# Kernel optimization log

Hardware: AMD Instinct MI355X
Metric: run time of the kernel (lower is better)

Reference implementation:

```python
import jax, jax.numpy as jnp
import numpy as np

B, S, H = 1, 1024, 2048          # batch, seq, hidden_size
I = 7168                          # intermediate_size
E = 8                             # num_local_experts
TOP_K = 2                         # num_experts_per_tok
R = int(I * H * 0.1 / (I + H))    # delta_low_rank = 159
SCALE = 0.02


def setup_inputs() -> dict:
    key = jax.random.key(0)
    ks = jax.random.split(key, 12)
    f = jnp.float32
    return {
        "x": jax.random.normal(ks[0], (B, S, H), dtype=f),
        "gate_w": jax.random.normal(ks[1], (E, H), dtype=f) * SCALE,
        "Wm1": jax.random.normal(ks[2], (I, H), dtype=f) * SCALE,  # Wmean1 (gate proj)
        "Wm2": jax.random.normal(ks[3], (H, I), dtype=f) * SCALE,  # Wmean2 (down proj)
        "Wm3": jax.random.normal(ks[4], (I, H), dtype=f) * SCALE,  # Wmean3 (up proj)
        "du1": jax.random.normal(ks[5], (E, I, R), dtype=f) * SCALE,
        "dv1": jax.random.normal(ks[6], (E, R, H), dtype=f) * SCALE,
        "du2": jax.random.normal(ks[7], (E, H, R), dtype=f) * SCALE,
        "dv2": jax.random.normal(ks[8], (E, R, I), dtype=f) * SCALE,
        "du3": jax.random.normal(ks[9], (E, I, R), dtype=f) * SCALE,
        "dv3": jax.random.normal(ks[10], (E, R, H), dtype=f) * SCALE,
    }


def reference(x, gate_w, Wm1, Wm2, Wm3, du1, dv1, du2, dv2, du3, dv3):
    b, s, h = x.shape
    hs = x.reshape(-1, h)                                  # [T, H]

    # --- router ---
    router_logits = hs @ gate_w.T                          # [T, E]
    probs = jax.nn.softmax(router_logits.astype(jnp.float32), axis=-1)
    top_w, top_i = jax.lax.top_k(probs, TOP_K)             # [T, K]
    top_w = top_w / jnp.sum(top_w, axis=-1, keepdims=True)
    # dense combine weights [T, E]: weight of expert e for token t (0 if not selected)
    comb = jnp.sum(jax.nn.one_hot(top_i, E, dtype=top_w.dtype) * top_w[..., None], axis=1)
    comb = comb.astype(hs.dtype)

    # --- shared mean weights (computed once per token) ---
    base_gate = hs @ Wm1.T                                 # [T, I]
    base_up = hs @ Wm3.T                                   # [T, I]

    # --- per-expert low-rank deltas ---
    t1 = jnp.einsum('th,erh->ter', hs, dv1)                # [T, E, R]
    gate = base_gate[:, None, :] + jnp.einsum('ter,eir->tei', t1, du1)  # [T, E, I]
    t3 = jnp.einsum('th,erh->ter', hs, dv3)
    up = base_up[:, None, :] + jnp.einsum('ter,eir->tei', t3, du3)      # [T, E, I]

    hmid = jax.nn.silu(gate) * up                          # [T, E, I]

    out = jnp.einsum('tei,hi->teh', hmid, Wm2)             # shared down proj
    t2 = jnp.einsum('tei,eri->ter', hmid, dv2)
    out = out + jnp.einsum('ter,ehr->teh', t2, du2)        # [T, E, H]

    final = jnp.einsum('te,teh->th', comb, out).reshape(b, s, h)
    return final, router_logits
```

## Files before the change

kernel.cpp:

```cpp
#include <hip/hip_runtime.h>

#define T_TOK 1024
#define H_DIM 2048
#define I_DIM 7168
#define E_NUM 8
#define R_RANK 159
#define RP 160
#define P_PAIRS 2048

#define CH_X    262144L
#define CH_W    1835008L
#define CH_DV13 325632L
#define CH_DV2  1139712L
#define CH_DU13 1146880L
#define CH_DU2  327680L

typedef __attribute__((ext_vector_type(8))) short short8;
typedef __attribute__((ext_vector_type(4))) float f32x4;

__device__ __forceinline__ ushort f2b(float f) {
  uint u = __float_as_uint(f);
  uint r = (u + 0x7FFFu + ((u >> 16) & 1u)) >> 16;
  return (ushort)r;
}
__device__ __forceinline__ float b2f(ushort u) {
  return __uint_as_float(((uint)u) << 16);
}
__device__ __forceinline__ short8 pack8(float4 a, float4 b) {
  short8 o;
  o[0] = (short)f2b(a.x); o[1] = (short)f2b(a.y); o[2] = (short)f2b(a.z); o[3] = (short)f2b(a.w);
  o[4] = (short)f2b(b.x); o[5] = (short)f2b(b.y); o[6] = (short)f2b(b.z); o[7] = (short)f2b(b.w);
  return o;
}
__device__ __forceinline__ short8 zero8() {
  short8 z;
#pragma unroll
  for (int q = 0; q < 8; ++q) z[q] = 0;
  return z;
}
__device__ __forceinline__ int swzofs(int row, int g) { return (g ^ ((row >> 1) & 3)) * 8; }

#define GLOAD(gptr, lptr) \
  __builtin_amdgcn_global_load_lds((const __attribute__((address_space(1))) void*)(gptr), \
                                   (__attribute__((address_space(3))) void*)(lptr), 16, 0, 0)

__global__ __launch_bounds__(256) void router_kernel(
    const float* __restrict__ x, const float* __restrict__ gw,
    float* __restrict__ logits, float* __restrict__ comb,
    int* __restrict__ sel_e, int* __restrict__ cnt) {
  int wave = threadIdx.x >> 6, lane = threadIdx.x & 63;
  int t = blockIdx.x * 4 + wave;
  const float* xr = x + (long)t * H_DIM;
  float acc[8] = {0.f,0.f,0.f,0.f,0.f,0.f,0.f,0.f};
  for (int h = lane * 4; h < H_DIM; h += 256) {
    const float4 xv = *(const float4*)&xr[h];
#pragma unroll
    for (int e = 0; e < 8; ++e) {
      const float4 gv = *(const float4*)&gw[e * H_DIM + h];
      acc[e] += xv.x * gv.x + xv.y * gv.y + xv.z * gv.z + xv.w * gv.w;
    }
  }
#pragma unroll
  for (int off = 32; off > 0; off >>= 1)
#pragma unroll
    for (int e = 0; e < 8; ++e) acc[e] += __shfl_down(acc[e], off);
  if (lane == 0) {
#pragma unroll
    for (int e = 0; e < 8; ++e) logits[(long)t * 8 + e] = acc[e];
    int i0 = 0;
    for (int e = 1; e < 8; ++e) if (acc[e] > acc[i0]) i0 = e;
    int i1 = (i0 == 0) ? 1 : 0;
    for (int e = 0; e < 8; ++e) if (e != i0 && acc[e] > acc[i1]) i1 = e;
    float ee = __expf(acc[i1] - acc[i0]);
    float w0 = 1.f / (1.f + ee), w1 = ee / (1.f + ee);
    for (int e = 0; e < 8; ++e) comb[t * 8 + e] = 0.f;
    comb[t * 8 + i0] = w0;
    comb[t * 8 + i1] = w1;
    sel_e[t * 2] = i0;
    sel_e[t * 2 + 1] = i1;
    atomicAdd(&cnt[i0], 1);
    atomicAdd(&cnt[i1], 1);
  }
}

__global__ void init_kernel(int* cnt, int* cursor) {
  int i = threadIdx.x;
  if (i < 8) { cnt[i] = 0; cursor[i] = 0; }
}

__global__ void scan_kernel(const int* cnt, int* seg) {
  if (threadIdx.x == 0) {
    int s = 0;
    for (int e = 0; e < 8; ++e) { seg[e] = s; s += cnt[e]; }
    seg[8] = s;
  }
}

__global__ void assign_kernel(const int* __restrict__ sel_e, const float* __restrict__ comb,
                              const int* __restrict__ seg, int* __restrict__ cursor,
                              int* __restrict__ tok, float* __restrict__ wrow,
                              int* __restrict__ row_of) {
  int t = blockIdx.x * blockDim.x + threadIdx.x;
  if (t >= T_TOK) return;
  for (int k = 0; k < 2; ++k) {
    int e = sel_e[t * 2 + k];
    int pos = atomicAdd(&cursor[e], 1);
    int row = seg[e] + pos;
    tok[row] = t;
    wrow[row] = comb[t * 8 + e];
    row_of[t * 2 + k] = row;
  }
}

__device__ __forceinline__ void castchunk(const float* __restrict__ s, ushort* __restrict__ d, long c) {
  const float4 a = *(const float4*)&s[c * 8];
  const float4 b = *(const float4*)&s[c * 8 + 4];
  *(short8*)&d[c * 8] = pack8(a, b);
}
__device__ __forceinline__ void padchunk(const float* __restrict__ s, ushort* __restrict__ d, long c) {
  long row = c / 20;
  int c0 = (int)(c % 20) * 8;
  short8 o;
#pragma unroll
  for (int j = 0; j < 8; ++j) {
    int cc = c0 + j;
    o[j] = (cc < R_RANK) ? (short)f2b(s[row * R_RANK + cc]) : (short)0;
  }
  *(short8*)&d[row * RP + c0] = o;
}

__global__ void megacast_kernel(
    const float* __restrict__ x, const float* __restrict__ Wm1, const float* __restrict__ Wm3,
    const float* __restrict__ dv1, const float* __restrict__ dv3,
    const float* __restrict__ du1, const float* __restrict__ du3, const float* __restrict__ du2,
    ushort* __restrict__ xb, ushort* __restrict__ w1b, ushort* __restrict__ w3b,
    ushort* __restrict__ dv1b, ushort* __restrict__ dv3b,
    ushort* __restrict__ du1b, ushort* __restrict__ du3b, ushort* __restrict__ du2b) {
  const long TOT = CH_W * 2 + CH_DU13 * 2 + CH_DU2 + CH_DV13 * 2 + CH_X;
  for (long c0 = (long)blockIdx.x * blockDim.x + threadIdx.x; c0 < TOT;
       c0 += (long)gridDim.x * blockDim.x) {
    long c = c0;
    if (c < CH_W)    { castchunk(Wm1, w1b, c); continue; }  c -= CH_W;
    if (c < CH_W)    { castchunk(Wm3, w3b, c); continue; }  c -= CH_W;
    if (c < CH_DU13) { padchunk(du1, du1b, c); continue; }  c -= CH_DU13;
    if (c < CH_DU13) { padchunk(du3, du3b, c); continue; }  c -= CH_DU13;
    if (c < CH_DU2)  { padchunk(du2, du2b, c); continue; }  c -= CH_DU2;
    if (c < CH_DV13) { castchunk(dv1, dv1b, c); continue; } c -= CH_DV13;
    if (c < CH_DV13) { castchunk(dv3, dv3b, c); continue; } c -= CH_DV13;
    castchunk(x, xb, c);
  }
}

__global__ void cast2_kernel(const float* __restrict__ Wm2, const float* __restrict__ dv2,
                             ushort* __restrict__ w2b, ushort* __restrict__ dv2b) {
  const long TOT = CH_W + CH_DV2;
  for (long c0 = (long)blockIdx.x * blockDim.x + threadIdx.x; c0 < TOT;
       c0 += (long)gridDim.x * blockDim.x) {
    long c = c0;
    if (c < CH_W) { castchunk(Wm2, w2b, c); continue; }
    c -= CH_W;
    castchunk(dv2, dv2b, c);
  }
}

__global__ void padcast8_kernel(const float* __restrict__ src, ushort* __restrict__ dst, long rows) {
  long n8 = rows * (RP / 8);
  long idx = (long)blockIdx.x * blockDim.x + threadIdx.x;
  long stride = (long)gridDim.x * blockDim.x;
  for (long i = idx; i < n8; i += stride) padchunk(src, dst, i);
}

__global__ void hcomb_kernel(const ushort* __restrict__ hmid, const int* __restrict__ row_of,
                             ushort* __restrict__ hc) {
  long idx = (long)blockIdx.x * blockDim.x + threadIdx.x;
  long total = (long)T_TOK * I_DIM / 8;
  if (idx >= total) return;
  long i = idx * 8;
  int t = (int)(i / I_DIM);
  int col = (int)(i % I_DIM);
  int r0 = row_of[t * 2], r1 = row_of[t * 2 + 1];
  const short8 a = *(const short8*)&hmid[(long)r0 * I_DIM + col];
  const short8 b = *(const short8*)&hmid[(long)r1 * I_DIM + col];
  short8 o;
#pragma unroll
  for (int j = 0; j < 8; ++j)
    o[j] = (short)f2b(b2f((ushort)a[j]) + b2f((ushort)b[j]));
  *(short8*)&hc[i] = o;
}

__global__ void finalfix_kernel(float* __restrict__ out, const ushort* __restrict__ delta,
                                const int* __restrict__ row_of) {
  long idx = (long)blockIdx.x * blockDim.x + threadIdx.x;
  long total = (long)T_TOK * H_DIM / 4;
  if (idx >= total) return;
  long i = idx * 4;
  int t = (int)(i / H_DIM);
  int col = (int)(i % H_DIM);
  int r0 = row_of[t * 2], r1 = row_of[t * 2 + 1];
  float4 d = *(float4*)&out[i];
  d.x += b2f(delta[(long)r0 * H_DIM + col + 0]) + b2f(delta[(long)r1 * H_DIM + col + 0]);
  d.y += b2f(delta[(long)r0 * H_DIM + col + 1]) + b2f(delta[(long)r1 * H_DIM + col + 1]);
  d.z += b2f(delta[(long)r0 * H_DIM + col + 2]) + b2f(delta[(long)r1 * H_DIM + col + 2]);
  d.w += b2f(delta[(long)r0 * H_DIM + col + 3]) + b2f(delta[(long)r1 * H_DIM + col + 3]);
  *(float4*)&out[i] = d;
}

__global__ void finalfixA_kernel(float* __restrict__ out, const float* __restrict__ dp,
                                 const ushort* __restrict__ delta, const int* __restrict__ row_of) {
  long idx = (long)blockIdx.x * blockDim.x + threadIdx.x;
  long total = (long)T_TOK * H_DIM / 4;
  if (idx >= total) return;
  long i = idx * 4;
  int t = (int)(i / H_DIM);
  int col = (int)(i % H_DIM);
  int r0 = row_of[t * 2], r1 = row_of[t * 2 + 1];
  const long plane = (long)T_TOK * H_DIM;
  float4 s = *(const float4*)&dp[i];
#pragma unroll
  for (int k = 1; k < 4; ++k) {
    const float4 q = *(const float4*)&dp[k * plane + i];
    s.x += q.x; s.y += q.y; s.z += q.z; s.w += q.w;
  }
  s.x += b2f(delta[(long)r0 * H_DIM + col + 0]) + b2f(delta[(long)r1 * H_DIM + col + 0]);
  s.y += b2f(delta[(long)r0 * H_DIM + col + 1]) + b2f(delta[(long)r1 * H_DIM + col + 1]);
  s.z += b2f(delta[(long)r0 * H_DIM + col + 2]) + b2f(delta[(long)r1 * H_DIM + col + 2]);
  s.w += b2f(delta[(long)r0 * H_DIM + col + 3]) + b2f(delta[(long)r1 * H_DIM + col + 3]);
  *(float4*)&out[i] = s;
}

template <int KS>
__global__ void reduce_cast_kernel(const float* __restrict__ P, long plane,
                                   ushort* __restrict__ out, long n) {
  long i = (long)blockIdx.x * blockDim.x + threadIdx.x;
  if (i >= n) return;
  float s = 0.f;
#pragma unroll
  for (int k = 0; k < KS; ++k) s += P[(long)k * plane + i];
  out[i] = f2b(s);
}

__global__ void reduce2_kernel(const float* __restrict__ p1, const float* __restrict__ p3,
                               ushort* __restrict__ t1g, ushort* __restrict__ t3g, long n) {
  long i = (long)blockIdx.x * blockDim.x + threadIdx.x;
  if (i >= 2 * n) return;
  const float* P = (i < n) ? p1 : p3;
  ushort* o = (i < n) ? t1g : t3g;
  long ii = (i < n) ? i : i - n;
  float s = 0.f;
#pragma unroll
  for (int k = 0; k < 8; ++k) s += P[(long)k * n + ii];
  o[ii] = f2b(s);
}


__device__ __forceinline__ void kloop32(
    const ushort* ar0, const ushort* ar1,
    const ushort* br0, const ushort* br1,
    int K, ushort* As, ushort* Bs,
    int tid, int lane, int wm, int wn, f32x4 acc[4][4]) {
  for (int k0 = 0; k0 < K; k0 += 32) {
    __syncthreads();
    GLOAD(ar0 + k0, &As[tid * 8]);
    GLOAD(ar1 + k0, &As[(256 + tid) * 8]);
    GLOAD(br0 + k0, &Bs[tid * 8]);
    GLOAD(br1 + k0, &Bs[(256 + tid) * 8]);
    __syncthreads();
    short8 av[4], bv[4];
#pragma unroll
    for (int mi = 0; mi < 4; ++mi) {
      int R = wm + mi * 16 + (lane & 15);
      av[mi] = *(const short8*)&As[R * 32 + swzofs(R, lane >> 4)];
    }
#pragma unroll
    for (int ni = 0; ni < 4; ++ni) {
      int R = wn + ni * 16 + (lane & 15);
      bv[ni] = *(const short8*)&Bs[R * 32 + swzofs(R, lane >> 4)];
    }
#pragma unroll
    for (int mi = 0; mi < 4; ++mi)
#pragma unroll
      for (int ni = 0; ni < 4; ++ni)
        acc[mi][ni] = __builtin_amdgcn_mfma_f32_16x16x32_bf16(av[mi], bv[ni], acc[mi][ni], 0, 0, 0);
  }
}

template <int NI>
__device__ __forceinline__ void kloop64t(
    const ushort* ar0, const ushort* ar1,
    const ushort* br0, const ushort* br1,
    int K, ushort* As, ushort* Bs,
    int tid, int lane, int wm, int wn, f32x4 acc[4][4]) {
  const int sub_r = tid >> 2;
  for (int k0 = 0; k0 < K; k0 += 64) {
    __syncthreads();
    GLOAD(ar0 + k0,      &As[tid * 8]);
    GLOAD(ar1 + k0,      &As[(256 + tid) * 8]);
    GLOAD(ar0 + k0 + 32, &As[4096 + tid * 8]);
    GLOAD(ar1 + k0 + 32, &As[4096 + (256 + tid) * 8]);
    if (NI == 4 || sub_r < 32) {
      GLOAD(br0 + k0,      &Bs[tid * 8]);
      GLOAD(br1 + k0,      &Bs[(256 + tid) * 8]);
      GLOAD(br0 + k0 + 32, &Bs[4096 + tid * 8]);
      GLOAD(br1 + k0 + 32, &Bs[4096 + (256 + tid) * 8]);
    }
    __syncthreads();
#pragma unroll
    for (int s = 0; s < 2; ++s) {
      short8 av[4], bv[NI];
#pragma unroll
      for (int mi = 0; mi < 4; ++mi) {
        int R = wm + mi * 16 + (lane & 15);
        av[mi] = *(const short8*)&As[s * 4096 + R * 32 + swzofs(R, lane >> 4)];
      }
#pragma unroll
      for (int ni = 0; ni < NI; ++ni) {
        int R = wn + ni * 16 + (lane & 15);
        bv[ni] = *(const short8*)&Bs[s * 4096 + R * 32 + swzofs(R, lane >> 4)];
      }
#pragma unroll
      for (int mi = 0; mi < 4; ++mi)
#pragma unroll
        for (int ni = 0; ni < NI; ++ni)
          acc[mi][ni] = __builtin_amdgcn_mfma_f32_16x16x32_bf16(av[mi], bv[ni], acc[mi][ni], 0, 0, 0);
    }
  }
}

__device__ __forceinline__ void epi_bf16(
    f32x4 acc[4][4], ushort* smem, int tid, int lane, int wm, int wn,
    int row0, int col0, int M, int Nvalid, int Npad, ushort* Cb, int ldc) {
  const int er = (lane >> 4) * 4, ec = lane & 15;
  __syncthreads();
#pragma unroll
  for (int mi = 0; mi < 4; ++mi)
#pragma unroll
    for (int ni = 0; ni < 4; ++ni)
#pragma unroll
      for (int j = 0; j < 4; ++j) {
        int rr = wm + mi * 16 + er + j;
        int c = wn + ni * 16 + ec;
        smem[rr * 128 + (c ^ ((rr & 7) << 3))] =
            (col0 + c < Nvalid) ? f2b(acc[mi][ni][j]) : (ushort)0;
      }
  __syncthreads();
  const int rl = tid >> 1, clb = (tid & 1) * 64;
  const int r = row0 + rl;
  if (r < M) {
    const int k8 = (rl & 7) << 3;
#pragma unroll
    for (int jj = 0; jj < 8; ++jj) {
      int cg = col0 + clb + jj * 8;
      if (cg < Npad) {
        short8 v = *(const short8*)&smem[rl * 128 + ((clb + jj * 8) ^ k8)];
        *(short8*)&Cb[(long)r * ldc + cg] = v;
      }
    }
  }
}


__global__ __launch_bounds__(256) void k_early(
    const ushort* __restrict__ xb, const ushort* __restrict__ w1b, const ushort* __restrict__ w3b,
    const ushort* __restrict__ dv1b, const ushort* __restrict__ dv3b,
    const int* __restrict__ tok, const int* __restrict__ seg, const int* __restrict__ cnt,
    ushort* __restrict__ bgate, ushort* __restrict__ bup,
    float* __restrict__ p1, float* __restrict__ p3) {
  __shared__ ushort smem[16384];
  ushort* As = smem;
  ushort* Bs = smem + 8192;
  const int b = blockIdx.x;
  const int tid = threadIdx.x;
  const int lane = tid & 63, wave = tid >> 6;
  const int wm = (wave >> 1) * 64, wn = (wave & 1) * 64;
  const int sub_r = tid >> 2, sub_c = swzofs(sub_r, tid & 3);

  if (b < 896) {
    const int z = b / 448, r448 = b % 448;
    const int xk = r448 % 56, yk = r448 / 56;
    const int row0 = yk * 128, col0 = xk * 128;
    const ushort* B = z ? w3b : w1b;
    ushort* C = z ? bup : bgate;
    const ushort* ar0 = xb + (long)(row0 + sub_r) * H_DIM + sub_c;
    const ushort* ar1 = xb + (long)(row0 + 64 + sub_r) * H_DIM + sub_c;
    const ushort* br0 = B + (long)(col0 + sub_r) * H_DIM + sub_c;
    const ushort* br1 = B + (long)(col0 + 64 + sub_r) * H_DIM + sub_c;
    f32x4 acc[4][4] = {};
    kloop64t<4>(ar0, ar1, br0, br1, H_DIM, As, Bs, tid, lane, wm, wn, acc);
    epi_bf16(acc, smem, tid, lane, wm, wn, row0, col0, T_TOK, I_DIM, I_DIM, C, I_DIM);
  } else {
    const int f = b - 896;
    const int xk = f & 1, yk = (f >> 1) & 7, zk = f >> 4;
    const int which = zk & 1;
    const int eks = zk >> 1;
    const int e = eks >> 3, ks = eks & 7;
    const int m0 = seg[e], M = cnt[e];
    const int row0 = yk * 128, col0 = xk * 128;
    if (row0 >= M) return;
    const int kbase = ks * 256;
    const ushort* Bsrc = (which ? dv3b : dv1b) + (long)e * R_RANK * H_DIM;
    float* P = which ? p3 : p1;
    int r0c = row0 + sub_r;      if (r0c > M - 1) r0c = M - 1;
    int r1c = row0 + 64 + sub_r; if (r1c > M - 1) r1c = M - 1;
    const ushort* ar0 = xb + (long)tok[m0 + r0c] * H_DIM + kbase + sub_c;
    const ushort* ar1 = xb + (long)tok[m0 + r1c] * H_DIM + kbase + sub_c;
    int q0 = col0 + sub_r;      if (q0 > R_RANK - 1) q0 = R_RANK - 1;
    int q1 = col0 + 64 + sub_r; if (q1 > R_RANK - 1) q1 = R_RANK - 1;
    const ushort* br0 = Bsrc + (long)q0 * H_DIM + kbase + sub_c;
    const ushort* br1 = Bsrc + (long)q1 * H_DIM + kbase + sub_c;
    f32x4 acc[4][4] = {};
    if (xk == 0)
      kloop64t<4>(ar0, ar1, br0, br1, 256, As, Bs, tid, lane, wm, wn, acc);
    else
      kloop64t<2>(ar0, ar1, br0, br1, 256, As, Bs, tid, lane, wm, wn, acc);
    const int er = (lane >> 4) * 4, ec = lane & 15;
    const long plane = (long)P_PAIRS * RP;
#pragma unroll
    for (int mi = 0; mi < 4; ++mi)
#pragma unroll
      for (int ni = 0; ni < 4; ++ni)
#pragma unroll
        for (int j = 0; j < 4; ++j) {
          int r = row0 + wm + mi * 16 + er + j;
          int c = col0 + wn + ni * 16 + ec;
          if (r < M && c < RP)
            P[(long)ks * plane + (long)(m0 + r) * RP + c] = (c < R_RANK) ? acc[mi][ni][j] : 0.f;
        }
  }
}

__global__ __launch_bounds__(256) void k_phase2(
    const ushort* __restrict__ hc, const ushort* __restrict__ w2b,
    const ushort* __restrict__ hmidg, const ushort* __restrict__ dv2b,
    const int* __restrict__ seg, const int* __restrict__ cnt,
    float* __restrict__ dp, float* __restrict__ p2) {
  __shared__ ushort smem[16384];
  ushort* As = smem;
  ushort* Bs = smem + 8192;
  const int tid = threadIdx.x;
  const int lane = tid & 63, wave = tid >> 6;
  const int wm = (wave >> 1) * 64, wn = (wave & 1) * 64;
  const int sub_r = tid >> 2, sub_c = swzofs(sub_r, tid & 3);
  const int er = (lane >> 4) * 4, ec = lane & 15;

  if (blockIdx.z < 4) {
    const int ks = blockIdx.z;
    const int kbase = ks * (I_DIM / 4);
    const int row0 = blockIdx.y * 128, col0 = blockIdx.x * 128;
    const ushort* ar0 = hc + (long)(row0 + sub_r) * I_DIM + kbase + sub_c;
    const ushort* ar1 = hc + (long)(row0 + 64 + sub_r) * I_DIM + kbase + sub_c;
    const ushort* br0 = w2b + (long)(col0 + sub_r) * I_DIM + kbase + sub_c;
    const ushort* br1 = w2b + (long)(col0 + 64 + sub_r) * I_DIM + kbase + sub_c;
    f32x4 acc[4][4] = {};
    kloop64t<4>(ar0, ar1, br0, br1, I_DIM / 4, As, Bs, tid, lane, wm, wn, acc);
    float* Pk = dp + (long)ks * T_TOK * H_DIM;
#pragma unroll
    for (int mi = 0; mi < 4; ++mi)
#pragma unroll
      for (int ni = 0; ni < 4; ++ni)
#pragma unroll
        for (int j = 0; j < 4; ++j) {
          int r = row0 + wm + mi * 16 + er + j;
          int c = col0 + wn + ni * 16 + ec;
          Pk[(long)r * H_DIM + c] = acc[mi][ni][j];
        }
  } else {
    const int f = (blockIdx.z - 4) * 128 + blockIdx.y * 16 + blockIdx.x;
    const int eks = f >> 4;
    const int e = eks >> 3, ks = eks & 7;
    const int rsub = f & 15;
    const int x2 = rsub & 1, y2 = rsub >> 1;
    const int m0 = seg[e], M = cnt[e];
    const int row0 = y2 * 128, col0 = x2 * 128;
    if (row0 >= M) return;
    const int kbase = ks * (I_DIM / 8);
    int r0c = row0 + sub_r;      if (r0c > M - 1) r0c = M - 1;
    int r1c = row0 + 64 + sub_r; if (r1c > M - 1) r1c = M - 1;
    const ushort* ar0 = hmidg + (long)(m0 + r0c) * I_DIM + kbase + sub_c;
    const ushort* ar1 = hmidg + (long)(m0 + r1c) * I_DIM + kbase + sub_c;
    int q0 = col0 + sub_r;      if (q0 > R_RANK - 1) q0 = R_RANK - 1;
    int q1 = col0 + 64 + sub_r; if (q1 > R_RANK - 1) q1 = R_RANK - 1;
    const ushort* br0 = dv2b + (long)e * R_RANK * I_DIM + (long)q0 * I_DIM + kbase + sub_c;
    const ushort* br1 = dv2b + (long)e * R_RANK * I_DIM + (long)q1 * I_DIM + kbase + sub_c;
    f32x4 acc[4][4] = {};
    if (x2 == 0)
      kloop64t<4>(ar0, ar1, br0, br1, I_DIM / 8, As, Bs, tid, lane, wm, wn, acc);
    else
      kloop64t<2>(ar0, ar1, br0, br1, I_DIM / 8, As, Bs, tid, lane, wm, wn, acc);
    const long plane = (long)P_PAIRS * RP;
#pragma unroll
    for (int mi = 0; mi < 4; ++mi)
#pragma unroll
      for (int ni = 0; ni < 4; ++ni)
#pragma unroll
        for (int j = 0; j < 4; ++j) {
          int r = row0 + wm + mi * 16 + er + j;
          int c = col0 + wn + ni * 16 + ec;
          if (r < M && c < RP)
            p2[(long)ks * plane + (long)(m0 + r) * RP + c] = (c < R_RANK) ? acc[mi][ni][j] : 0.f;
        }
  }
}

__global__ __launch_bounds__(256) void k_delta(
    const ushort* __restrict__ t2g, const ushort* __restrict__ du2b,
    const int* __restrict__ seg, const int* __restrict__ cnt,
    ushort* __restrict__ deltab) {
  __shared__ ushort smem[16384];
  ushort* As = smem;
  ushort* Bs = smem + 4096;
  const int e = blockIdx.z;
  const int m0 = seg[e], M = cnt[e];
  const int row0 = blockIdx.y * 128, col0 = blockIdx.x * 128;
  if (row0 >= M) return;
  const int tid = threadIdx.x;
  const int lane = tid & 63, wave = tid >> 6;
  const int wm = (wave >> 1) * 64, wn = (wave & 1) * 64;
  const int sub_r = tid >> 2, sub_c = swzofs(sub_r, tid & 3);
  int r0c = row0 + sub_r;      if (r0c > M - 1) r0c = M - 1;
  int r1c = row0 + 64 + sub_r; if (r1c > M - 1) r1c = M - 1;
  const ushort* ar0 = t2g + (long)(m0 + r0c) * RP + sub_c;
  const ushort* ar1 = t2g + (long)(m0 + r1c) * RP + sub_c;
  const ushort* br0 = du2b + (long)e * H_DIM * RP + (long)(col0 + sub_r) * RP + sub_c;
  const ushort* br1 = du2b + (long)e * H_DIM * RP + (long)(col0 + 64 + sub_r) * RP + sub_c;
  f32x4 acc[4][4] = {};
  kloop32(ar0, ar1, br0, br1, RP, As, Bs, tid, lane, wm, wn, acc);
  epi_bf16(acc, smem, tid, lane, wm, wn, row0, col0, M, H_DIM, H_DIM,
           deltab + (long)m0 * H_DIM, H_DIM);
}

__global__ __launch_bounds__(256) void gemm_hmid(
    const ushort* __restrict__ t1g, const ushort* __restrict__ t3g,
    const ushort* __restrict__ du1b, const ushort* __restrict__ du3b,
    const ushort* __restrict__ bgate, const ushort* __restrict__ bup,
    const int* __restrict__ tok, const float* __restrict__ wrow,
    const int* __restrict__ seg, const int* __restrict__ cnt,
    ushort* __restrict__ hmid) {
  __shared__ ushort smem[16384];
  ushort* As1 = smem;
  ushort* As3 = smem + 4096;
  ushort* Bs1 = smem + 8192;
  ushort* Bs3 = smem + 12288;
  int e = blockIdx.z;
  int m0 = seg[e], M = cnt[e];
  if ((int)(blockIdx.y * 128) >= M) return;
  const ushort* A1 = t1g + (long)m0 * RP;
  const ushort* A3 = t3g + (long)m0 * RP;
  const ushort* B1 = du1b + (long)e * I_DIM * RP;
  const ushort* B3 = du3b + (long)e * I_DIM * RP;
  tok += m0; wrow += m0;
  ushort* H = hmid + (long)m0 * I_DIM;

  const int tid = threadIdx.x;
  const int lane = tid & 63, wave = tid >> 6;
  const int wm = (wave >> 1) * 64, wn = (wave & 1) * 64;
  const int row0 = blockIdx.y * 128, col0 = blockIdx.x * 128;
  const int sub_r = tid >> 2;
  const int sub_c = swzofs(sub_r, tid & 3);

  const ushort *a1r[2], *a3r[2], *b1r[2], *b3r[2];
#pragma unroll
  for (int p = 0; p < 2; ++p) {
    int r = row0 + p * 64 + sub_r; if (r > M - 1) r = M - 1;
    a1r[p] = A1 + (long)r * RP + sub_c;
    a3r[p] = A3 + (long)r * RP + sub_c;
    int q = col0 + p * 64 + sub_r; if (q > I_DIM - 1) q = I_DIM - 1;
    b1r[p] = B1 + (long)q * RP + sub_c;
    b3r[p] = B3 + (long)q * RP + sub_c;
  }

  f32x4 acc1[4][4] = {}, acc3[4][4] = {};

  for (int k0 = 0; k0 < RP; k0 += 32) {
    __syncthreads();
#pragma unroll
    for (int p = 0; p < 2; ++p) {
      GLOAD(a1r[p] + k0, &As1[(p * 256 + tid) * 8]);
      GLOAD(a3r[p] + k0, &As3[(p * 256 + tid) * 8]);
      GLOAD(b1r[p] + k0, &Bs1[(p * 256 + tid) * 8]);
      GLOAD(b3r[p] + k0, &Bs3[(p * 256 + tid) * 8]);
    }
    __syncthreads();

    short8 av1[4], av3[4], bv1[4], bv3[4];
#pragma unroll
    for (int mi = 0; mi < 4; ++mi) {
      int R = wm + mi * 16 + (lane & 15);
      int o = R * 32 + swzofs(R, lane >> 4);
      av1[mi] = *(const short8*)&As1[o];
      av3[mi] = *(const short8*)&As3[o];
    }
#pragma unroll
    for (int ni = 0; ni < 4; ++ni) {
      int R = wn + ni * 16 + (lane & 15);
      int o = R * 32 + swzofs(R, lane >> 4);
      bv1[ni] = *(const short8*)&Bs1[o];
      bv3[ni] = *(const short8*)&Bs3[o];
    }
#pragma unroll
    for (int mi = 0; mi < 4; ++mi)
#pragma unroll
      for (int ni = 0; ni < 4; ++ni) {
        acc1[mi][ni] = __builtin_amdgcn_mfma_f32_16x16x32_bf16(av1[mi], bv1[ni], acc1[mi][ni], 0, 0, 0);
        acc3[mi][ni] = __builtin_amdgcn_mfma_f32_16x16x32_bf16(av3[mi], bv3[ni], acc3[mi][ni], 0, 0, 0);
      }
  }

  const int er = (lane >> 4) * 4;
  const int ec = lane & 15;
  __syncthreads();
  ushort* Cs = smem;
#pragma unroll
  for (int mi = 0; mi < 4; ++mi)
#pragma unroll
    for (int ni = 0; ni < 4; ++ni)
#pragma unroll
      for (int j = 0; j < 4; ++j) {
        int rr = wm + mi * 16 + er + j;
        int c = wn + ni * 16 + ec;
        Cs[rr * 128 + (c ^ ((rr & 7) << 3))] = f2b(acc1[mi][ni][j]);
      }
  __syncthreads();
  const int rl = tid >> 1;
  const int clb = (tid & 1) * 64;
  const int r = row0 + rl;
  const bool rok = (r < M);
  const int t = rok ? tok[r] : 0;
  const float w = rok ? wrow[r] : 0.f;
  const int k8 = (rl & 7) << 3;
  uint svp[32];
#pragma unroll
  for (int jj = 0; jj < 8; ++jj) {
    short8 gb = zero8();
    if (rok) gb = *(const short8*)&bgate[(long)t * I_DIM + col0 + clb + jj * 8];
    short8 gv = *(const short8*)&Cs[rl * 128 + ((clb + jj * 8) ^ k8)];
#pragma unroll
    for (int q = 0; q < 8; q += 2) {
      float g0 = b2f((ushort)gv[q]) + b2f((ushort)gb[q]);
      float g1 = b2f((ushort)gv[q + 1]) + b2f((ushort)gb[q + 1]);
      float s0 = g0 / (1.f + __expf(-g0));
      float s1 = g1 / (1.f + __expf(-g1));
      svp[jj * 4 + q / 2] = (uint)f2b(s0) | ((uint)f2b(s1) << 16);
    }
  }
  __syncthreads();
#pragma unroll
  for (int mi = 0; mi < 4; ++mi)
#pragma unroll
    for (int ni = 0; ni < 4; ++ni)
#pragma unroll
      for (int j = 0; j < 4; ++j) {
        int rr = wm + mi * 16 + er + j;
        int c = wn + ni * 16 + ec;
        Cs[rr * 128 + (c ^ ((rr & 7) << 3))] = f2b(acc3[mi][ni][j]);
      }
  __syncthreads();
#pragma unroll
  for (int jj = 0; jj < 8; ++jj) {
    short8 ub = zero8();
    if (rok) ub = *(const short8*)&bup[(long)t * I_DIM + col0 + clb + jj * 8];
    short8 uv = *(const short8*)&Cs[rl * 128 + ((clb + jj * 8) ^ k8)];
    short8 o;
#pragma unroll
    for (int q = 0; q < 8; q += 2) {
      uint sp = svp[jj * 4 + q / 2];
      float u0 = b2f((ushort)uv[q]) + b2f((ushort)ub[q]);
      float u1 = b2f((ushort)uv[q + 1]) + b2f((ushort)ub[q + 1]);
      o[q]     = (short)f2b(w * b2f((ushort)(sp & 0xFFFFu)) * u0);
      o[q + 1] = (short)f2b(w * b2f((ushort)(sp >> 16)) * u1);
    }
    if (rok) *(short8*)&H[(long)r * I_DIM + col0 + clb + jj * 8] = o;
  }
}

template <int AF32, int BF32, int CBF16, int PEREXP, int AMAP>
__global__ __launch_bounds__(256) void gemm_f(
    const void* __restrict__ Ap, int lda,
    const void* __restrict__ Bp, int ldb, long Bstride,
    int M, int N, int K, int Npad,
    float* __restrict__ Cf, ushort* __restrict__ Cb, int ldc,
    const int* __restrict__ tok, const int* __restrict__ seg, const int* __restrict__ cnt) {
  __shared__ ushort smem[16384];
  ushort* As = smem;
  ushort* Bs = smem + 4096;
  const float* Af = (const float*)Ap;
  const ushort* Ab = (const ushort*)Ap;
  const float* Bf = (const float*)Bp;
  const ushort* Bb = (const ushort*)Bp;
  const int* amap = tok;
  if (PEREXP) {
    int e = blockIdx.z;
    int m0 = seg[e];
    M = cnt[e];
    if ((int)(blockIdx.y * 128) >= M) return;
    if (AMAP) {
      amap = tok + m0;
    } else {
      if (AF32) Af += (long)m0 * lda; else Ab += (long)m0 * lda;
    }
    if (BF32) Bf += (long)e * Bstride; else Bb += (long)e * Bstride;
    if (CBF16) Cb += (long)m0 * ldc; else Cf += (long)m0 * ldc;
  }
  const int tid = threadIdx.x;
  const int lane = tid & 63, wave = tid >> 6;
  const int wm = (wave >> 1) * 64, wn = (wave & 1) * 64;
  const int row0 = blockIdx.y * 128, col0 = blockIdx.x * 128;
  const int sub_r = tid >> 2;
  const int sub_c = (tid & 3) * 8;

  const float* afrow[2]; const ushort* abrow[2];
  const float* bfrow[2]; const ushort* bbrow[2];
#pragma unroll
  for (int p = 0; p < 2; ++p) {
    int r = row0 + p * 64 + sub_r; if (r > M - 1) r = M - 1;
    if (AMAP) r = amap[r];
    if (AF32) afrow[p] = Af + (long)r * lda + sub_c;
    else      abrow[p] = Ab + (long)r * lda + sub_c;
    int q = col0 + p * 64 + sub_r; if (q > N - 1) q = N - 1;
    if (BF32) bfrow[p] = Bf + (long)q * ldb + sub_c;
    else      bbrow[p] = Bb + (long)q * ldb + sub_c;
  }

  f32x4 acc[4][4] = {};

  for (int k0 = 0; k0 < K; k0 += 32) {
    float4 a0[2], a1[2], b0[2], b1[2];
    if (AF32) {
#pragma unroll
      for (int p = 0; p < 2; ++p) {
        a0[p] = *(const float4*)(afrow[p] + k0);
        a1[p] = *(const float4*)(afrow[p] + k0 + 4);
      }
    }
    if (BF32) {
#pragma unroll
      for (int p = 0; p < 2; ++p) {
        b0[p] = *(const float4*)(bfrow[p] + k0);
        b1[p] = *(const float4*)(bfrow[p] + k0 + 4);
      }
    }
    __syncthreads();
#pragma unroll
    for (int p = 0; p < 2; ++p) {
      if (AF32) {
        *(short8*)&As[(p * 256 + tid) * 8] = pack8(a0[p], a1[p]);
      } else {
        GLOAD(abrow[p] + k0, &As[(p * 256 + tid) * 8]);
      }
      if (BF32) {
        *(short8*)&Bs[(p * 256 + tid) * 8] = pack8(b0[p], b1[p]);
      } else {
        GLOAD(bbrow[p] + k0, &Bs[(p * 256 + tid) * 8]);
      }
    }
    __syncthreads();

    short8 av[4], bv[4];
#pragma unroll
    for (int mi = 0; mi < 4; ++mi)
      av[mi] = *(const short8*)&As[(wm + mi * 16 + (lane & 15)) * 32 + (lane >> 4) * 8];
#pragma unroll
    for (int ni = 0; ni < 4; ++ni)
      bv[ni] = *(const short8*)&Bs[(wn + ni * 16 + (lane & 15)) * 32 + (lane >> 4) * 8];
#pragma unroll
    for (int mi = 0; mi < 4; ++mi)
#pragma unroll
      for (int ni = 0; ni < 4; ++ni)
        acc[mi][ni] = __builtin_amdgcn_mfma_f32_16x16x32_bf16(av[mi], bv[ni], acc[mi][ni], 0, 0, 0);
  }

  const int er = (lane >> 4) * 4;
  const int ec = lane & 15;
  if (CBF16) {
    __syncthreads();
    ushort* Cs = smem;
#pragma unroll
    for (int mi = 0; mi < 4; ++mi)
#pragma unroll
      for (int ni = 0; ni < 4; ++ni)
#pragma unroll
        for (int j = 0; j < 4; ++j) {
          int rr = wm + mi * 16 + er + j;
          int c = wn + ni * 16 + ec;
          Cs[rr * 128 + (c ^ ((rr & 7) << 3))] =
              (col0 + c < N) ? f2b(acc[mi][ni][j]) : (ushort)0;
        }
    __syncthreads();
    const int rl = tid >> 1;
    const int clb = (tid & 1) * 64;
    const int r = row0 + rl;
    if (r < M) {
      const int k8 = (rl & 7) << 3;
#pragma unroll
      for (int jj = 0; jj < 8; ++jj) {
        int cg = col0 + clb + jj * 8;
        if (cg < Npad) {
          short8 v = *(const short8*)&Cs[rl * 128 + ((clb + jj * 8) ^ k8)];
          *(short8*)&Cb[(long)r * ldc + cg] = v;
        }
      }
    }
  } else {
#pragma unroll
    for (int mi = 0; mi < 4; ++mi)
#pragma unroll
      for (int ni = 0; ni < 4; ++ni)
#pragma unroll
        for (int j = 0; j < 4; ++j) {
          int r = row0 + wm + mi * 16 + er + j;
          int c = col0 + wn + ni * 16 + ec;
          if (r < M && c < Npad)
            Cf[(long)r * ldc + c] = (c < N) ? acc[mi][ni][j] : 0.f;
        }
  }
}

extern "C" void kernel_launch(void* const* d_in, const int* in_sizes, int n_in,
                              void* d_out, int out_size, void* d_ws, size_t ws_size,
                              hipStream_t stream) {
  const float* x   = (const float*)d_in[0];
  const float* gw  = (const float*)d_in[1];
  const float* Wm1 = (const float*)d_in[2];
  const float* Wm2 = (const float*)d_in[3];
  const float* Wm3 = (const float*)d_in[4];
  const float* du1 = (const float*)d_in[5];
  const float* dv1 = (const float*)d_in[6];
  const float* du2 = (const float*)d_in[7];
  const float* dv2 = (const float*)d_in[8];
  const float* du3 = (const float*)d_in[9];
  const float* dv3 = (const float*)d_in[10];

  float* out_final  = (float*)d_out;
  float* out_logits = out_final + (long)T_TOK * H_DIM;

  char* p = (char*)d_ws;
  auto alloc = [&](size_t bytes) {
    char* r = p;
    p += (bytes + 255) & ~(size_t)255;
    return r;
  };

  float* comb   = (float*)alloc((size_t)T_TOK * E_NUM * 4);
  float* wrow   = (float*)alloc((size_t)P_PAIRS * 4);
  int* cnt      = (int*)alloc(64);
  int* cursor   = (int*)alloc(64);
  int* seg      = (int*)alloc(64);
  int* sel_e    = (int*)alloc((size_t)T_TOK * 2 * 4);
  int* tok      = (int*)alloc((size_t)P_PAIRS * 4);
  int* row_of   = (int*)alloc((size_t)T_TOK * 2 * 4);
  ushort* bgate_b = (ushort*)alloc((size_t)T_TOK * I_DIM * 2);
  ushort* bup_b   = (ushort*)alloc((size_t)T_TOK * I_DIM * 2);
  ushort* hmidg   = (ushort*)alloc((size_t)P_PAIRS * I_DIM * 2);
  ushort* t1g     = (ushort*)alloc((size_t)P_PAIRS * RP * 2);
  ushort* t3g     = (ushort*)alloc((size_t)P_PAIRS * RP * 2);
  ushort* t2g     = (ushort*)alloc((size_t)P_PAIRS * RP * 2);
  ushort* du1b    = (ushort*)alloc((size_t)E_NUM * I_DIM * RP * 2);
  ushort* du3b    = (ushort*)alloc((size_t)E_NUM * I_DIM * RP * 2);
  ushort* du2b    = (ushort*)alloc((size_t)E_NUM * H_DIM * RP * 2);
  size_t needed_B = (size_t)(p - (char*)d_ws);
  ushort* xb   = (ushort*)alloc((size_t)T_TOK * H_DIM * 2);
  ushort* w1b  = (ushort*)alloc((size_t)I_DIM * H_DIM * 2);
  ushort* w3b  = (ushort*)alloc((size_t)I_DIM * H_DIM * 2);
  ushort* dv1b = (ushort*)alloc((size_t)E_NUM * R_RANK * H_DIM * 2);
  ushort* dv3b = (ushort*)alloc((size_t)E_NUM * R_RANK * H_DIM * 2);
  size_t needed_A = (size_t)(p - (char*)d_ws);
  ushort* w2b_d  = (ushort*)alloc((size_t)I_DIM * H_DIM * 2);
  ushort* dv2b_d = (ushort*)alloc((size_t)E_NUM * R_RANK * I_DIM * 2);
  size_t needed_A2 = (size_t)(p - (char*)d_ws);

  ushort* hc     = bgate_b;
  ushort* deltab = bup_b;

  if (ws_size < needed_B) return;
  const bool planA  = (ws_size >= needed_A);
  const bool planA2 = (ws_size >= needed_A2);

  dim3 blk(256);

  init_kernel<<<1, 64, 0, stream>>>(cnt, cursor);
  router_kernel<<<T_TOK / 4, 256, 0, stream>>>(x, gw, out_logits, comb, sel_e, cnt);
  scan_kernel<<<1, 64, 0, stream>>>(cnt, seg);
  assign_kernel<<<4, 256, 0, stream>>>(sel_e, comb, seg, cursor, tok, wrow, row_of);

  if (planA) {
    ushort* w2b  = planA2 ? w2b_d  : w1b;
    ushort* dv2b = planA2 ? dv2b_d : w3b;

    megacast_kernel<<<2048, 256, 0, stream>>>(x, Wm1, Wm3, dv1, dv3, du1, du3, du2,
                                              xb, w1b, w3b, dv1b, dv3b, du1b, du3b, du2b);
    if (planA2)
      cast2_kernel<<<1024, 256, 0, stream>>>(Wm2, dv2, w2b, dv2b);

    float* p1 = (float*)hmidg;
    float* p3 = p1 + (long)8 * P_PAIRS * RP;
    k_early<<<2944, blk, 0, stream>>>(xb, w1b, w3b, dv1b, dv3b, tok, seg, cnt,
                                      bgate_b, bup_b, p1, p3);
    reduce2_kernel<<<2560, 256, 0, stream>>>(p1, p3, t1g, t3g, (long)P_PAIRS * RP);

    if (!planA2)
      cast2_kernel<<<1024, 256, 0, stream>>>(Wm2, dv2, w2b, dv2b);

    gemm_hmid<<<dim3(I_DIM / 128, 8, E_NUM), blk, 0, stream>>>(
        t1g, t3g, du1b, du3b, bgate_b, bup_b, tok, wrow, seg, cnt, hmidg);

    hcomb_kernel<<<(int)(((long)T_TOK * I_DIM / 8 + 255) / 256), 256, 0, stream>>>(hmidg, row_of, hc);

    float* dp = (float*)du1b;
    float* p2 = (float*)bup_b;
    k_phase2<<<dim3(H_DIM / 128, 8, 12), blk, 0, stream>>>(
        hc, w2b, hmidg, dv2b, seg, cnt, dp, p2);
    reduce_cast_kernel<8><<<1280, 256, 0, stream>>>(p2, (long)P_PAIRS * RP, t2g, (long)P_PAIRS * RP);

    k_delta<<<dim3(H_DIM / 128, 8, E_NUM), blk, 0, stream>>>(t2g, du2b, seg, cnt, deltab);

    finalfixA_kernel<<<2048, 256, 0, stream>>>(out_final, dp, deltab, row_of);
  } else {
    padcast8_kernel<<<4480, 256, 0, stream>>>(du1, du1b, (long)E_NUM * I_DIM);
    padcast8_kernel<<<4480, 256, 0, stream>>>(du3, du3b, (long)E_NUM * I_DIM);
    padcast8_kernel<<<1280, 256, 0, stream>>>(du2, du2b, (long)E_NUM * H_DIM);
    gemm_f<1, 1, 1, 0, 0><<<dim3(I_DIM / 128, T_TOK / 128, 1), blk, 0, stream>>>(
        x, H_DIM, Wm1, H_DIM, 0L, T_TOK, I_DIM, H_DIM, I_DIM,
        nullptr, bgate_b, I_DIM, nullptr, nullptr, nullptr);
    gemm_f<1, 1, 1, 0, 0><<<dim3(I_DIM / 128, T_TOK / 128, 1), blk, 0, stream>>>(
        x, H_DIM, Wm3, H_DIM, 0L, T_TOK, I_DIM, H_DIM, I_DIM,
        nullptr, bup_b, I_DIM, nullptr, nullptr, nullptr);
    gemm_f<1, 1, 1, 1, 1><<<dim3(2, 8, E_NUM), blk, 0, stream>>>(
        x, H_DIM, dv1, H_DIM, (long)R_RANK * H_DIM, 0, R_RANK, H_DIM, RP,
        nullptr, t1g, RP, tok, seg, cnt);
    gemm_f<1, 1, 1, 1, 1><<<dim3(2, 8, E_NUM), blk, 0, stream>>>(
        x, H_DIM, dv3, H_DIM, (long)R_RANK * H_DIM, 0, R_RANK, H_DIM, RP,
        nullptr, t3g, RP, tok, seg, cnt);
    gemm_hmid<<<dim3(I_DIM / 128, 8, E_NUM), blk, 0, stream>>>(
        t1g, t3g, du1b, du3b, bgate_b, bup_b, tok, wrow, seg, cnt, hmidg);
    hcomb_kernel<<<(int)(((long)T_TOK * I_DIM / 8 + 255) / 256), 256, 0, stream>>>(hmidg, row_of, hc);
    gemm_f<0, 1, 0, 0, 0><<<dim3(H_DIM / 128, T_TOK / 128, 1), blk, 0, stream>>>(
        hc, I_DIM, Wm2, I_DIM, 0L, T_TOK, H_DIM, I_DIM, H_DIM,
        out_final, nullptr, H_DIM, nullptr, nullptr, nullptr);
    gemm_f<0, 1, 1, 1, 0><<<dim3(2, 8, E_NUM), blk, 0, stream>>>(
        hmidg, I_DIM, dv2, I_DIM, (long)R_RANK * I_DIM, 0, R_RANK, I_DIM, RP,
        nullptr, t2g, RP, tok, seg, cnt);
    gemm_f<0, 0, 1, 1, 0><<<dim3(H_DIM / 128, 8, E_NUM), blk, 0, stream>>>(
        t2g, RP, du2b, RP, (long)H_DIM * RP, 0, H_DIM, RP, H_DIM,
        nullptr, deltab, H_DIM, tok, seg, cnt);
    finalfix_kernel<<<(int)(((long)T_TOK * H_DIM / 4 + 255) / 256), 256, 0, stream>>>(
        out_final, deltab, row_of);
  }
}
```

Before: 480.1 us.

## Merge routing setup kernels and fold Wm2/dv2 cast into early GEMM launch

Replaces the init, scan and assign kernels and the global atomic counts with a single-block setup kernel that does the histogram, prefix scan and row assignment using shared-memory atomics. It also removes the separate cast2 launch and appends 512 extra blocks to k_early that cast Wm2 and dv2 to bf16, so the cast can overlap with the GEMM tiles. This cuts several tiny launches and serialization points. The trade-off is that a single block handles the setup, and the cast blocks compete with the GEMM blocks for bandwidth and CUs.

```diff
diff --git a/kernel.cpp b/kernel.cpp
--- a/kernel.cpp
+++ b/kernel.cpp
@@ -47,7 +47,7 @@
 __global__ __launch_bounds__(256) void router_kernel(
     const float* __restrict__ x, const float* __restrict__ gw,
     float* __restrict__ logits, float* __restrict__ comb,
-    int* __restrict__ sel_e, int* __restrict__ cnt) {
+    int* __restrict__ sel_e) {
   int wave = threadIdx.x >> 6, lane = threadIdx.x & 63;
   int t = blockIdx.x * 4 + wave;
   const float* xr = x + (long)t * H_DIM;
@@ -78,37 +78,38 @@
     comb[t * 8 + i1] = w1;
     sel_e[t * 2] = i0;
     sel_e[t * 2 + 1] = i1;
-    atomicAdd(&cnt[i0], 1);
-    atomicAdd(&cnt[i1], 1);
-  }
-}
-
-__global__ void init_kernel(int* cnt, int* cursor) {
-  int i = threadIdx.x;
-  if (i < 8) { cnt[i] = 0; cursor[i] = 0; }
-}
-
-__global__ void scan_kernel(const int* cnt, int* seg) {
-  if (threadIdx.x == 0) {
+  }
+}
+
+__global__ __launch_bounds__(256) void setup_kernel(
+    const int* __restrict__ sel_e, const float* __restrict__ comb,
+    int* __restrict__ cnt, int* __restrict__ seg,
+    int* __restrict__ tok, float* __restrict__ wrow, int* __restrict__ row_of) {
+  __shared__ int sc[8];
+  __shared__ int sseg[8];
+  __shared__ int scur[8];
+  const int tid = threadIdx.x;
+  if (tid < 8) sc[tid] = 0;
+  __syncthreads();
+  for (int i = tid; i < T_TOK * 2; i += 256) atomicAdd(&sc[sel_e[i]], 1);
+  __syncthreads();
+  if (tid == 0) {
     int s = 0;
-    for (int e = 0; e < 8; ++e) { seg[e] = s; s += cnt[e]; }
+    for (int e = 0; e < 8; ++e) { cnt[e] = sc[e]; seg[e] = s; sseg[e] = s; s += sc[e]; }
     seg[8] = s;
   }
-}
-
-__global__ void assign_kernel(const int* __restrict__ sel_e, const float* __restrict__ comb,
-                              const int* __restrict__ seg, int* __restrict__ cursor,
-                              int* __restrict__ tok, float* __restrict__ wrow,
-                              int* __restrict__ row_of) {
-  int t = blockIdx.x * blockDim.x + threadIdx.x;
-  if (t >= T_TOK) return;
-  for (int k = 0; k < 2; ++k) {
-    int e = sel_e[t * 2 + k];
-    int pos = atomicAdd(&cursor[e], 1);
-    int row = seg[e] + pos;
-    tok[row] = t;
-    wrow[row] = comb[t * 8 + e];
-    row_of[t * 2 + k] = row;
+  if (tid < 8) scur[tid] = 0;
+  __syncthreads();
+  for (int t = tid; t < T_TOK; t += 256) {
+#pragma unroll
+    for (int k = 0; k < 2; ++k) {
+      int e = sel_e[t * 2 + k];
+      int pos = atomicAdd(&scur[e], 1);
+      int row = sseg[e] + pos;
+      tok[row] = t;
+      wrow[row] = comb[t * 8 + e];
+      row_of[t * 2 + k] = row;
+    }
   }
 }
 
@@ -364,7 +365,9 @@
     const ushort* __restrict__ dv1b, const ushort* __restrict__ dv3b,
     const int* __restrict__ tok, const int* __restrict__ seg, const int* __restrict__ cnt,
     ushort* __restrict__ bgate, ushort* __restrict__ bup,
-    float* __restrict__ p1, float* __restrict__ p3) {
+    float* __restrict__ p1, float* __restrict__ p3,
+    const float* __restrict__ Wm2, const float* __restrict__ dv2,
+    ushort* __restrict__ w2b, ushort* __restrict__ dv2b, int docast) {
   __shared__ ushort smem[16384];
   ushort* As = smem;
   ushort* Bs = smem + 8192;
@@ -387,7 +390,7 @@
     f32x4 acc[4][4] = {};
     kloop64t<4>(ar0, ar1, br0, br1, H_DIM, As, Bs, tid, lane, wm, wn, acc);
     epi_bf16(acc, smem, tid, lane, wm, wn, row0, col0, T_TOK, I_DIM, I_DIM, C, I_DIM);
-  } else {
+  } else if (b < 2944) {
     const int f = b - 896;
     const int xk = f & 1, yk = (f >> 1) & 7, zk = f >> 4;
     const int which = zk & 1;
@@ -425,6 +428,14 @@
           if (r < M && c < RP)
             P[(long)ks * plane + (long)(m0 + r) * RP + c] = (c < R_RANK) ? acc[mi][ni][j] : 0.f;
         }
+  } else if (docast) {
+    const long TOT = CH_W + CH_DV2;
+    for (long c0 = (long)(b - 2944) * 256 + tid; c0 < TOT; c0 += 512L * 256L) {
+      long c = c0;
+      if (c < CH_W) { castchunk(Wm2, w2b, c); continue; }
+      c -= CH_W;
+      castchunk(dv2, dv2b, c);
+    }
   }
 }
 
@@ -842,7 +853,6 @@
   float* comb   = (float*)alloc((size_t)T_TOK * E_NUM * 4);
   float* wrow   = (float*)alloc((size_t)P_PAIRS * 4);
   int* cnt      = (int*)alloc(64);
-  int* cursor   = (int*)alloc(64);
   int* seg      = (int*)alloc(64);
   int* sel_e    = (int*)alloc((size_t)T_TOK * 2 * 4);
   int* tok      = (int*)alloc((size_t)P_PAIRS * 4);
@@ -876,10 +886,8 @@
 
   dim3 blk(256);
 
-  init_kernel<<<1, 64, 0, stream>>>(cnt, cursor);
-  router_kernel<<<T_TOK / 4, 256, 0, stream>>>(x, gw, out_logits, comb, sel_e, cnt);
-  scan_kernel<<<1, 64, 0, stream>>>(cnt, seg);
-  assign_kernel<<<4, 256, 0, stream>>>(sel_e, comb, seg, cursor, tok, wrow, row_of);
+  router_kernel<<<T_TOK / 4, 256, 0, stream>>>(x, gw, out_logits, comb, sel_e);
+  setup_kernel<<<1, 256, 0, stream>>>(sel_e, comb, cnt, seg, tok, wrow, row_of);
 
   if (planA) {
     ushort* w2b  = planA2 ? w2b_d  : w1b;
@@ -887,13 +895,12 @@
 
     megacast_kernel<<<2048, 256, 0, stream>>>(x, Wm1, Wm3, dv1, dv3, du1, du3, du2,
                                               xb, w1b, w3b, dv1b, dv3b, du1b, du3b, du2b);
-    if (planA2)
-      cast2_kernel<<<1024, 256, 0, stream>>>(Wm2, dv2, w2b, dv2b);
 
     float* p1 = (float*)hmidg;
     float* p3 = p1 + (long)8 * P_PAIRS * RP;
-    k_early<<<2944, blk, 0, stream>>>(xb, w1b, w3b, dv1b, dv3b, tok, seg, cnt,
-                                      bgate_b, bup_b, p1, p3);
+    k_early<<<3456, blk, 0, stream>>>(xb, w1b, w3b, dv1b, dv3b, tok, seg, cnt,
+                                      bgate_b, bup_b, p1, p3,
+                                      Wm2, dv2, w2b, dv2b, planA2 ? 1 : 0);
     reduce2_kernel<<<2560, 256, 0, stream>>>(p1, p3, t1g, t3g, (long)P_PAIRS * RP);
 
     if (!planA2)
```

After: 435.2 us, median of 2. 1.1x faster.
